# Optimization experiments

Hardware: AMD Instinct MI355X
Metric: run time of the kernel (lower is better)

The kernel has to match this reference:

```python
import jax, jax.numpy as jnp
import numpy as np

B, S, H, SSZ, IN = 1024, 100, 128, 100, 2


def _gru(x, h, Wih, Whh, bih, bhh):
    # PyTorch GRU cell: gates ordered (reset, update, new)
    gx = x @ Wih.T + bih
    gh = h @ Whh.T + bhh
    xr, xz, xn = jnp.split(gx, 3, axis=-1)
    hr, hz, hn = jnp.split(gh, 3, axis=-1)
    r = jax.nn.sigmoid(xr + hr)
    z = jax.nn.sigmoid(xz + hz)
    n = jnp.tanh(xn + r * hn)
    return (1.0 - z) * n + z * h


def _attn(inst_h, rnn_out, W, v):
    # inst_h: [B,S,H], rnn_out: [B,H] -> softmax attention weights [B,S]
    h = jnp.concatenate([inst_h, jnp.broadcast_to(rnn_out[:, None, :], inst_h.shape)], axis=-1)
    s = jax.nn.relu(jnp.einsum('bsk,kh->bsh', h, W)) @ v
    return jax.nn.softmax(s, axis=1)


def setup_inputs() -> dict:
    key = jax.random.key(0)
    k = jax.random.split(key, 32)
    p = lambda i, shape, sc=0.05: sc * jax.random.normal(k[i], shape, jnp.float32)
    instance = jax.random.uniform(k[0], (B, S, IN), jnp.float32)
    # solutions must be per-row permutations of node indices
    solution_1 = jnp.argsort(jax.random.uniform(k[1], (B, S)), axis=1).astype(jnp.int32)
    solution_2 = jnp.argsort(jax.random.uniform(k[2], (B, S)), axis=1).astype(jnp.int32)
    eps = jax.random.normal(k[3], (B, SSZ), jnp.float32)
    return dict(
        instance=instance, solution_1=solution_1, solution_2=solution_2, eps=eps,
        emb_i_W=p(4, (H, IN)), emb_i_b=jnp.zeros(H, jnp.float32),
        emb_r_W=p(5, (H, IN)), emb_r_b=jnp.zeros(H, jnp.float32),
        attn_W=p(6, (2 * H, H)), attn_v=p(7, (H,)),
        gru_Wih=p(8, (3 * H, H)), gru_Whh=p(9, (3 * H, H)),
        gru_bih=jnp.zeros(3 * H, jnp.float32), gru_bhh=jnp.zeros(3 * H, jnp.float32),
        grud_Wih=p(10, (3 * H, 2 * H)), grud_Whh=p(11, (3 * H, H)),
        grud_bih=jnp.zeros(3 * H, jnp.float32), grud_bhh=jnp.zeros(3 * H, jnp.float32),
        enc_fc1_W=p(12, (SSZ, H)), enc_fc1_b=jnp.zeros(SSZ, jnp.float32),
        enc_fc2_W=p(13, (SSZ, H)), enc_fc2_b=jnp.zeros(SSZ, jnp.float32),
        ptr_W=p(14, (2 * H, H)), ptr_v=p(15, (H,)),
        pfc1_W=p(16, (2 * H, 2 * H + SSZ)), pfc1_b=jnp.zeros(2 * H, jnp.float32),
        pfc2_W=p(17, (H, 2 * H)), pfc2_b=jnp.zeros(H, jnp.float32),
    )


def reference(instance, solution_1, solution_2, eps,
              emb_i_W, emb_i_b, emb_r_W, emb_r_b, attn_W, attn_v,
              gru_Wih, gru_Whh, gru_bih, gru_bhh,
              grud_Wih, grud_Whh, grud_bih, grud_bhh,
              enc_fc1_W, enc_fc1_b, enc_fc2_W, enc_fc2_b,
              ptr_W, ptr_v, pfc1_W, pfc1_b, pfc2_W, pfc2_b):
    b_idx = jnp.arange(B)
    inst_h = instance @ emb_i_W.T + emb_i_b  # [B,S,H]
    emb_r = lambda x: x @ emb_r_W.T + emb_r_b
    take = lambda ptr: instance[b_idx, ptr]  # gather node coords [B,IN]

    # ---------------- Encoder ----------------
    def enc_step(carry, ptr):
        h1, h2, ref_h = carry
        h1 = _gru(ref_h, h1, gru_Wih, gru_Whh, gru_bih, gru_bhh)
        a = _attn(inst_h, h1, attn_W, attn_v)
        context = jnp.einsum('bs,bsh->bh', a, inst_h)
        ref_h = emb_r(take(ptr))
        rnn_in = jnp.concatenate([ref_h, context], axis=-1)  # [B,2H]
        h2 = _gru(rnn_in, h2, grud_Wih, grud_Whh, grud_bih, grud_bhh)
        return (h1, h2, ref_h), None

    z0 = jnp.zeros((B, H), instance.dtype)
    ref_h0 = emb_r(take(solution_1[:, 0]))
    (_, h2, _), _ = jax.lax.scan(enc_step, (z0, z0, ref_h0), solution_1[:, 1:].T)
    mu = h2 @ enc_fc1_W.T + enc_fc1_b
    log_var = h2 @ enc_fc2_W.T + enc_fc2_b
    Z = mu + eps * jnp.exp(0.5 * log_var)

    # ---------------- Decoder (teacher forcing) ----------------
    mask0 = jnp.ones((B, S), instance.dtype).at[b_idx, solution_2[:, 0]].set(0.0)

    def dec_step(carry, ptr):
        h1, ref_in, mask = carry
        ref_h = emb_r(ref_in)
        h1 = _gru(ref_h, h1, gru_Wih, gru_Whh, gru_bih, gru_bhh)
        a = _attn(inst_h, h1, attn_W, attn_v)
        context = jnp.einsum('bs,bsh->bh', a, inst_h)
        fc_in = jnp.concatenate([context, Z, ref_h], axis=-1)  # [B, 2H+SSZ]
        fc_out = (fc_in @ pfc1_W.T + pfc1_b) @ pfc2_W.T + pfc2_b  # no activation, as in torch
        hcat = jnp.concatenate([inst_h, jnp.broadcast_to(fc_out[:, None, :], inst_h.shape)], axis=-1)
        logits = jnp.tanh(jnp.einsum('bsk,kh->bsh', hcat, ptr_W)) @ ptr_v  # [B,S]
        probs = jax.nn.softmax(logits + jnp.log(mask), axis=1)
        logp = jnp.log(probs[b_idx, ptr])
        pred = jnp.argmax(probs, axis=1)
        mask = mask.at[b_idx, ptr].set(0.0)  # tsp.update_mask: mark chosen node visited
        return (h1, take(ptr), mask), (pred, logp)

    init = (z0, take(solution_2[:, 0]), mask0)
    _, (preds, logps) = jax.lax.scan(dec_step, init, solution_2[:, 1:].T)
    tour_idx = jnp.concatenate([solution_2[:, :1], preds.T.astype(solution_2.dtype)], axis=1)
    tour_logp = logps.T  # [B, S-1]
    return (mu, log_var, Z, tour_idx, tour_logp)
```

## Files before the change

kernel.cpp:

```cpp
#include <hip/hip_runtime.h>
#include <math.h>

static constexpr int NB  = 1024;
static constexpr int NS  = 100;
static constexpr int NH  = 128;
static constexpr int GPB = 2;
static constexpr int NTHR = 256;
static constexpr int NBLK = NB / GPB;

static constexpr int OUT_MU = 0;
static constexpr int OUT_LV = NB * NS;
static constexpr int OUT_Z  = 2 * NB * NS;
static constexpr int OUT_TI = 3 * NB * NS;
static constexpr int OUT_LP = 4 * NB * NS;

#define NEGF (-3.4e38f)

template<int C4>
__device__ __forceinline__ void dot2x3f(const float* __restrict__ wr0,
        const float* __restrict__ wr1, const float* __restrict__ wr2,
        const float* __restrict__ x0, const float* __restrict__ x1,
        float& r00, float& r01, float& r10, float& r11, float& r20, float& r21)
{
    const float4* W0 = reinterpret_cast<const float4*>(wr0);
    const float4* W1 = reinterpret_cast<const float4*>(wr1);
    const float4* W2 = reinterpret_cast<const float4*>(wr2);
    const float4* X0 = reinterpret_cast<const float4*>(x0);
    const float4* X1 = reinterpret_cast<const float4*>(x1);
    float a00 = 0.f, a01 = 0.f, a10 = 0.f, a11 = 0.f, a20 = 0.f, a21 = 0.f;
    #pragma unroll 8
    for (int c = 0; c < C4; ++c) {
        float4 u0 = W0[c], u1 = W1[c], u2 = W2[c];
        float4 v0 = X0[c], v1 = X1[c];
        a00 = fmaf(u0.x, v0.x, a00); a00 = fmaf(u0.y, v0.y, a00); a00 = fmaf(u0.z, v0.z, a00); a00 = fmaf(u0.w, v0.w, a00);
        a01 = fmaf(u0.x, v1.x, a01); a01 = fmaf(u0.y, v1.y, a01); a01 = fmaf(u0.z, v1.z, a01); a01 = fmaf(u0.w, v1.w, a01);
        a10 = fmaf(u1.x, v0.x, a10); a10 = fmaf(u1.y, v0.y, a10); a10 = fmaf(u1.z, v0.z, a10); a10 = fmaf(u1.w, v0.w, a10);
        a11 = fmaf(u1.x, v1.x, a11); a11 = fmaf(u1.y, v1.y, a11); a11 = fmaf(u1.z, v1.z, a11); a11 = fmaf(u1.w, v1.w, a11);
        a20 = fmaf(u2.x, v0.x, a20); a20 = fmaf(u2.y, v0.y, a20); a20 = fmaf(u2.z, v0.z, a20); a20 = fmaf(u2.w, v0.w, a20);
        a21 = fmaf(u2.x, v1.x, a21); a21 = fmaf(u2.y, v1.y, a21); a21 = fmaf(u2.z, v1.z, a21); a21 = fmaf(u2.w, v1.w, a21);
    }
    r00 = a00; r01 = a01; r10 = a10; r11 = a11; r20 = a20; r21 = a21;
}

template<int C4>
__device__ __forceinline__ void dot2f(const float* __restrict__ w,
        const float* __restrict__ x0, const float* __restrict__ x1, float& r0, float& r1)
{
    const float4* W = reinterpret_cast<const float4*>(w);
    const float4* X0 = reinterpret_cast<const float4*>(x0);
    const float4* X1 = reinterpret_cast<const float4*>(x1);
    float a0 = 0.f, a1 = 0.f;
    #pragma unroll 8
    for (int c = 0; c < C4; ++c) {
        float4 u = W[c];
        float4 v0 = X0[c], v1 = X1[c];
        a0 = fmaf(u.x, v0.x, a0); a0 = fmaf(u.y, v0.y, a0); a0 = fmaf(u.z, v0.z, a0); a0 = fmaf(u.w, v0.w, a0);
        a1 = fmaf(u.x, v1.x, a1); a1 = fmaf(u.y, v1.y, a1); a1 = fmaf(u.z, v1.z, a1); a1 = fmaf(u.w, v1.w, a1);
    }
    r0 = a0; r1 = a1;
}

template<int C4>
__device__ __forceinline__ void dot1f(const float* __restrict__ w,
        const float* __restrict__ x0, float& r0)
{
    const float4* W = reinterpret_cast<const float4*>(w);
    const float4* X0 = reinterpret_cast<const float4*>(x0);
    float a0 = 0.f;
    #pragma unroll 8
    for (int c = 0; c < C4; ++c) {
        float4 u = W[c];
        float4 v0 = X0[c];
        a0 = fmaf(u.x, v0.x, a0); a0 = fmaf(u.y, v0.y, a0); a0 = fmaf(u.z, v0.z, a0); a0 = fmaf(u.w, v0.w, a0);
    }
    r0 = a0;
}

template<int C4>
__device__ __forceinline__ double dotwd(const float* __restrict__ w, const float* __restrict__ x)
{
    const float4* W = reinterpret_cast<const float4*>(w);
    double a = 0.0;
    #pragma unroll 8
    for (int c = 0; c < C4; ++c) {
        float4 u = W[c];
        const float* p = x + 4 * c;
        a = fma((double)u.x, (double)p[0], a);
        a = fma((double)u.y, (double)p[1], a);
        a = fma((double)u.z, (double)p[2], a);
        a = fma((double)u.w, (double)p[3], a);
    }
    return a;
}

__device__ __forceinline__ void gruc(const float* __restrict__ bih, const float* __restrict__ bhh,
        const float* __restrict__ pa, const float* __restrict__ pb, float* __restrict__ h, int j)
{
    double r = 1.0 / (1.0 + exp(-(((double)pa[j]        + (double)bih[j])        + ((double)pb[j]        + (double)bhh[j]))));
    double z = 1.0 / (1.0 + exp(-(((double)pa[NH + j]   + (double)bih[NH + j])   + ((double)pb[NH + j]   + (double)bhh[NH + j]))));
    double n = tanh(((double)pa[2*NH + j] + (double)bih[2*NH + j]) + r * ((double)pb[2*NH + j] + (double)bhh[2*NH + j]));
    h[j] = (float)((1.0 - z) * n + z * (double)h[j]);
}

__global__ __launch_bounds__(NTHR) void vae_v14(
    const float* __restrict__ instance, const int* __restrict__ sol1,
    const int* __restrict__ sol2, const float* __restrict__ eps,
    const float* __restrict__ emb_i_W, const float* __restrict__ emb_i_b,
    const float* __restrict__ emb_r_W, const float* __restrict__ emb_r_b,
    const float* __restrict__ attn_W, const float* __restrict__ attn_v,
    const float* __restrict__ gru_Wih, const float* __restrict__ gru_Whh,
    const float* __restrict__ gru_bih, const float* __restrict__ gru_bhh,
    const float* __restrict__ grud_Wih, const float* __restrict__ grud_Whh,
    const float* __restrict__ grud_bih, const float* __restrict__ grud_bhh,
    const float* __restrict__ efc1_W, const float* __restrict__ efc1_b,
    const float* __restrict__ efc2_W, const float* __restrict__ efc2_b,
    const float* __restrict__ ptr_W, const float* __restrict__ ptr_v,
    const float* __restrict__ pfc1_W, const float* __restrict__ pfc1_b,
    const float* __restrict__ pfc2_W, const float* __restrict__ pfc2_b,
    float* __restrict__ out)
{
    __shared__ float  s_x[GPB][360];
    __shared__ float  s_h1[GPB][NH], s_h2[GPB][NH], s_fco[GPB][NH];
    __shared__ float  s_fch[GPB][256];
    __shared__ float  s_pa[GPB][3 * NH], s_pb[GPB][3 * NH];
    __shared__ double s_qh[GPB][NH];
    __shared__ double s_qpA[GPB][NH], s_qpB[GPB][NH];
    __shared__ double2 dAa[NH], dAp[NH];
    __shared__ double dAba[NH], dAbp[NH];
    __shared__ float  s_lg[GPB][NS], s_a[GPB][NS];
    __shared__ float  s_c0[GPB][NS], s_c1[GPB][NS], s_msk[GPB][NS];
    __shared__ float  t_wi0[NH], t_wi1[NH], t_bi[NH];
    __shared__ float  t_wr0[NH], t_wr1[NH], t_br[NH];
    __shared__ float  t_va[NH], t_vp[NH];
    __shared__ float  t_gbih[3*NH], t_gbhh[3*NH], t_dbih[3*NH], t_dbhh[3*NH];
    __shared__ float  t_p1b[256], t_p2b[NH];
    __shared__ int    s_sol1[GPB][NS], s_sol2[GPB][NS];
    __shared__ float  s_red[GPB][2];
    __shared__ double s_redd[GPB][2];
    __shared__ int    s_ri[GPB][2];
    __shared__ float  s_rc0[GPB], s_rc1[GPB];

    const int tid = threadIdx.x;
    const int bbase = blockIdx.x * GPB;
    const int j = tid & (NH - 1);
    const int half = tid >> 7;
    const int g = half;
    const int lane = tid & 63;
    const int wid = (tid >> 6) & 1;

    if (tid < NH) {
        t_wi0[tid] = emb_i_W[2*tid]; t_wi1[tid] = emb_i_W[2*tid+1]; t_bi[tid] = emb_i_b[tid];
        t_wr0[tid] = emb_r_W[2*tid]; t_wr1[tid] = emb_r_W[2*tid+1]; t_br[tid] = emb_r_b[tid];
        t_va[tid] = attn_v[tid]; t_vp[tid] = ptr_v[tid];
        t_p2b[tid] = pfc2_b[tid];
    }
    t_p1b[tid] = pfc1_b[tid];
    for (int i = tid; i < 3 * NH; i += NTHR) {
        t_gbih[i] = gru_bih[i]; t_gbhh[i] = gru_bhh[i];
        t_dbih[i] = grud_bih[i]; t_dbhh[i] = grud_bhh[i];
    }
    for (int i = tid; i < GPB * NS; i += NTHR) {
        int gg = i / NS, s = i - gg * NS;
        s_c0[gg][s] = instance[(size_t)((bbase + gg) * NS + s) * 2 + 0];
        s_c1[gg][s] = instance[(size_t)((bbase + gg) * NS + s) * 2 + 1];
        s_sol1[gg][s] = sol1[(bbase + gg) * NS + s];
        s_sol2[gg][s] = sol2[(bbase + gg) * NS + s];
    }
    s_h1[g][j] = 0.f;
    s_h2[g][j] = 0.f;
    __syncthreads();
    {
        const float* Wm = (half == 0) ? attn_W : ptr_W;
        double a0 = 0.0, a1 = 0.0, ab = 0.0;
        for (int k = 0; k < NH; ++k) {
            double wv = (double)Wm[(size_t)k * NH + j];
            a0 = fma((double)t_wi0[k], wv, a0);
            a1 = fma((double)t_wi1[k], wv, a1);
            ab = fma((double)t_bi[k],  wv, ab);
        }
        if (half == 0) { dAa[j].x = a0; dAa[j].y = a1; dAba[j] = ab; }
        else           { dAp[j].x = a0; dAp[j].y = a1; dAbp[j] = ab; }
    }
    {
        int sp = s_sol1[g][0];
        s_x[g][j] = fmaf(s_c0[g][sp], t_wr0[j], fmaf(s_c1[g][sp], t_wr1[j], t_br[j]));
    }
    __syncthreads();

    for (int t = 1; t < NS; ++t) {
        if (half == 0) {
            float a00,a01,a10,a11,a20,a21;
            dot2x3f<32>(gru_Wih + (size_t)j * NH, gru_Wih + (size_t)(NH + j) * NH,
                        gru_Wih + (size_t)(2*NH + j) * NH, s_x[0], s_x[1],
                        a00,a01,a10,a11,a20,a21);
            s_pa[0][j] = a00;        s_pa[1][j] = a01;
            s_pa[0][NH + j] = a10;   s_pa[1][NH + j] = a11;
            s_pa[0][2*NH + j] = a20; s_pa[1][2*NH + j] = a21;
        } else {
            float a00,a01,a10,a11,a20,a21;
            dot2x3f<32>(gru_Whh + (size_t)j * NH, gru_Whh + (size_t)(NH + j) * NH,
                        gru_Whh + (size_t)(2*NH + j) * NH, s_h1[0], s_h1[1],
                        a00,a01,a10,a11,a20,a21);
            s_pb[0][j] = a00;        s_pb[1][j] = a01;
            s_pb[0][NH + j] = a10;   s_pb[1][NH + j] = a11;
            s_pb[0][2*NH + j] = a20; s_pb[1][2*NH + j] = a21;
        }
        __syncthreads();
        gruc(t_gbih, t_gbhh, s_pa[g], s_pb[g], s_h1[g], j);
        __syncthreads();
        {
            const float* col = attn_W + (size_t)NH * NH + j;
            const int k0 = half * 64;
            double a00=0.0,a01=0.0,a02=0.0,a03=0.0;
            double a10=0.0,a11=0.0,a12=0.0,a13=0.0;
            #pragma unroll 8
            for (int k = 0; k < 64; k += 4) {
                float w0 = col[(size_t)(k0+k+0) * NH];
                float w1 = col[(size_t)(k0+k+1) * NH];
                float w2 = col[(size_t)(k0+k+2) * NH];
                float w3 = col[(size_t)(k0+k+3) * NH];
                float4 h0 = *reinterpret_cast<const float4*>(&s_h1[0][k0+k]);
                float4 h1v = *reinterpret_cast<const float4*>(&s_h1[1][k0+k]);
                a00 = fma((double)w0, (double)h0.x, a00);
                a01 = fma((double)w1, (double)h0.y, a01);
                a02 = fma((double)w2, (double)h0.z, a02);
                a03 = fma((double)w3, (double)h0.w, a03);
                a10 = fma((double)w0, (double)h1v.x, a10);
                a11 = fma((double)w1, (double)h1v.y, a11);
                a12 = fma((double)w2, (double)h1v.z, a12);
                a13 = fma((double)w3, (double)h1v.w, a13);
            }
            if (half == 0) { s_qpA[0][j] = (a00+a01)+(a02+a03); s_qpA[1][j] = (a10+a11)+(a12+a13); }
            else           { s_qpB[0][j] = (a00+a01)+(a02+a03); s_qpB[1][j] = (a10+a11)+(a12+a13); }
        }
        __syncthreads();
        s_qh[g][j] = dAba[j] + (s_qpA[g][j] + s_qpB[g][j]);
        __syncthreads();
        if (j < NS) {
            double c00 = (double)s_c0[g][j], c10 = (double)s_c1[g][j];
            double acc0 = 0.0, acc1 = 0.0, acc2 = 0.0, acc3 = 0.0;
            #pragma unroll 4
            for (int h = 0; h < NH; h += 4) {
                double2 A0 = dAa[h+0], A1 = dAa[h+1], A2 = dAa[h+2], A3 = dAa[h+3];
                double p0 = fma(c00, A0.x, fma(c10, A0.y, s_qh[g][h+0]));
                double p1 = fma(c00, A1.x, fma(c10, A1.y, s_qh[g][h+1]));
                double p2 = fma(c00, A2.x, fma(c10, A2.y, s_qh[g][h+2]));
                double p3 = fma(c00, A3.x, fma(c10, A3.y, s_qh[g][h+3]));
                acc0 = fma(fmax(p0, 0.0), (double)t_va[h+0], acc0);
                acc1 = fma(fmax(p1, 0.0), (double)t_va[h+1], acc1);
                acc2 = fma(fmax(p2, 0.0), (double)t_va[h+2], acc2);
                acc3 = fma(fmax(p3, 0.0), (double)t_va[h+3], acc3);
            }
            s_lg[g][j] = (float)(((acc0 + acc1) + (acc2 + acc3)));
        }
        __syncthreads();
        {
            float a = s_lg[g][lane];
            float b = (lane + 64 < NS) ? s_lg[g][lane + 64] : NEGF;
            float m = fmaxf(a, b);
            m = fmaxf(m, __shfl_xor(m, 32)); m = fmaxf(m, __shfl_xor(m, 16));
            m = fmaxf(m, __shfl_xor(m, 8));  m = fmaxf(m, __shfl_xor(m, 4));
            m = fmaxf(m, __shfl_xor(m, 2));  m = fmaxf(m, __shfl_xor(m, 1));
            float fv = 0.f;
            if (j < NS) { fv = (float)exp((double)s_lg[g][j] - (double)m); s_a[g][j] = fv; }
            double ps = (double)fv;
            ps += __shfl_xor(ps, 32); ps += __shfl_xor(ps, 16);
            ps += __shfl_xor(ps, 8);  ps += __shfl_xor(ps, 4);
            ps += __shfl_xor(ps, 2);  ps += __shfl_xor(ps, 1);
            if (lane == 0) s_redd[g][wid] = ps;
        }
        __syncthreads();
        if (j < NS) {
            double se = s_redd[g][0] + s_redd[g][1];
            s_a[g][j] = (float)((double)s_a[g][j] / se);
        }
        __syncthreads();
        {
            float w0 = t_wi0[j], w1 = t_wi1[j], bb = t_bi[j];
            double a0 = 0.0, a1 = 0.0, a2 = 0.0, a3 = 0.0;
            #pragma unroll 5
            for (int s = 0; s < NS; s += 4) {
                float ih0 = fmaf(s_c0[g][s+0], w0, fmaf(s_c1[g][s+0], w1, bb));
                float ih1 = fmaf(s_c0[g][s+1], w0, fmaf(s_c1[g][s+1], w1, bb));
                float ih2 = fmaf(s_c0[g][s+2], w0, fmaf(s_c1[g][s+2], w1, bb));
                float ih3 = fmaf(s_c0[g][s+3], w0, fmaf(s_c1[g][s+3], w1, bb));
                a0 += (double)s_a[g][s+0] * (double)ih0;
                a1 += (double)s_a[g][s+1] * (double)ih1;
                a2 += (double)s_a[g][s+2] * (double)ih2;
                a3 += (double)s_a[g][s+3] * (double)ih3;
            }
            s_x[g][NH + j] = (float)(((a0 + a1) + (a2 + a3)));
            int sp = s_sol1[g][t];
            s_x[g][j] = fmaf(s_c0[g][sp], t_wr0[j], fmaf(s_c1[g][sp], t_wr1[j], t_br[j]));
        }
        __syncthreads();
        if (half == 0) {
            float a00,a01,a10,a11,a20,a21;
            dot2x3f<64>(grud_Wih + (size_t)j * 256, grud_Wih + (size_t)(NH + j) * 256,
                        grud_Wih + (size_t)(2*NH + j) * 256, s_x[0], s_x[1],
                        a00,a01,a10,a11,a20,a21);
            s_pa[0][j] = a00;        s_pa[1][j] = a01;
            s_pa[0][NH + j] = a10;   s_pa[1][NH + j] = a11;
            s_pa[0][2*NH + j] = a20; s_pa[1][2*NH + j] = a21;
        } else {
            float a00,a01,a10,a11,a20,a21;
            dot2x3f<32>(grud_Whh + (size_t)j * NH, grud_Whh + (size_t)(NH + j) * NH,
                        grud_Whh + (size_t)(2*NH + j) * NH, s_h2[0], s_h2[1],
                        a00,a01,a10,a11,a20,a21);
            s_pb[0][j] = a00;        s_pb[1][j] = a01;
            s_pb[0][NH + j] = a10;   s_pb[1][NH + j] = a11;
            s_pb[0][2*NH + j] = a20; s_pb[1][2*NH + j] = a21;
        }
        __syncthreads();
        gruc(t_dbih, t_dbhh, s_pa[g], s_pb[g], s_h2[g], j);
        __syncthreads();
    }

    for (int idx = tid; idx < GPB * NS; idx += NTHR) {
        int gg = idx / NS, s = idx - gg * NS, b = bbase + gg;
        double mu = dotwd<32>(efc1_W + (size_t)s * NH, s_h2[gg]) + (double)efc1_b[s];
        double lv = dotwd<32>(efc2_W + (size_t)s * NH, s_h2[gg]) + (double)efc2_b[s];
        double z  = mu + (double)eps[(size_t)b * NS + s] * exp(0.5 * lv);
        out[OUT_MU + b * NS + s] = (float)mu;
        out[OUT_LV + b * NS + s] = (float)lv;
        out[OUT_Z  + b * NS + s] = (float)z;
        s_x[gg][NH + s] = (float)z;
    }
    for (int i = tid; i < GPB * NS; i += NTHR) {
        int gg = i / NS, s = i - gg * NS;
        s_msk[gg][s] = 1.f;
    }
    s_h1[g][j] = 0.f;
    __syncthreads();
    if (tid < GPB) {
        int b = bbase + tid;
        int s0 = s_sol2[tid][0];
        s_msk[tid][s0] = 0.f;
        s_rc0[tid] = s_c0[tid][s0];
        s_rc1[tid] = s_c1[tid][s0];
        out[OUT_TI + b * NS + 0] = (float)s0;
    }
    __syncthreads();

    for (int t = 1; t < NS; ++t) {
        s_x[g][228 + j] = fmaf(s_rc0[g], t_wr0[j], fmaf(s_rc1[g], t_wr1[j], t_br[j]));
        __syncthreads();
        if (half == 0) {
            float a00,a01,a10,a11,a20,a21;
            dot2x3f<32>(gru_Wih + (size_t)j * NH, gru_Wih + (size_t)(NH + j) * NH,
                        gru_Wih + (size_t)(2*NH + j) * NH, s_x[0]+228, s_x[1]+228,
                        a00,a01,a10,a11,a20,a21);
            s_pa[0][j] = a00;        s_pa[1][j] = a01;
            s_pa[0][NH + j] = a10;   s_pa[1][NH + j] = a11;
            s_pa[0][2*NH + j] = a20; s_pa[1][2*NH + j] = a21;
        } else {
            float a00,a01,a10,a11,a20,a21;
            dot2x3f<32>(gru_Whh + (size_t)j * NH, gru_Whh + (size_t)(NH + j) * NH,
                        gru_Whh + (size_t)(2*NH + j) * NH, s_h1[0], s_h1[1],
                        a00,a01,a10,a11,a20,a21);
            s_pb[0][j] = a00;        s_pb[1][j] = a01;
            s_pb[0][NH + j] = a10;   s_pb[1][NH + j] = a11;
            s_pb[0][2*NH + j] = a20; s_pb[1][2*NH + j] = a21;
        }
        __syncthreads();
        gruc(t_gbih, t_gbhh, s_pa[g], s_pb[g], s_h1[g], j);
        __syncthreads();
        {
            const float* col = attn_W + (size_t)NH * NH + j;
            const int k0 = half * 64;
            double a00=0.0,a01=0.0,a02=0.0,a03=0.0;
            double a10=0.0,a11=0.0,a12=0.0,a13=0.0;
            #pragma unroll 8
            for (int k = 0; k < 64; k += 4) {
                float w0 = col[(size_t)(k0+k+0) * NH];
                float w1 = col[(size_t)(k0+k+1) * NH];
                float w2 = col[(size_t)(k0+k+2) * NH];
                float w3 = col[(size_t)(k0+k+3) * NH];
                float4 h0 = *reinterpret_cast<const float4*>(&s_h1[0][k0+k]);
                float4 h1v = *reinterpret_cast<const float4*>(&s_h1[1][k0+k]);
                a00 = fma((double)w0, (double)h0.x, a00);
                a01 = fma((double)w1, (double)h0.y, a01);
                a02 = fma((double)w2, (double)h0.z, a02);
                a03 = fma((double)w3, (double)h0.w, a03);
                a10 = fma((double)w0, (double)h1v.x, a10);
                a11 = fma((double)w1, (double)h1v.y, a11);
                a12 = fma((double)w2, (double)h1v.z, a12);
                a13 = fma((double)w3, (double)h1v.w, a13);
            }
            if (half == 0) { s_qpA[0][j] = (a00+a01)+(a02+a03); s_qpA[1][j] = (a10+a11)+(a12+a13); }
            else           { s_qpB[0][j] = (a00+a01)+(a02+a03); s_qpB[1][j] = (a10+a11)+(a12+a13); }
        }
        __syncthreads();
        s_qh[g][j] = dAba[j] + (s_qpA[g][j] + s_qpB[g][j]);
        __syncthreads();
        if (j < NS) {
            double c00 = (double)s_c0[g][j], c10 = (double)s_c1[g][j];
            double acc0 = 0.0, acc1 = 0.0, acc2 = 0.0, acc3 = 0.0;
            #pragma unroll 4
            for (int h = 0; h < NH; h += 4) {
                double2 A0 = dAa[h+0], A1 = dAa[h+1], A2 = dAa[h+2], A3 = dAa[h+3];
                double p0 = fma(c00, A0.x, fma(c10, A0.y, s_qh[g][h+0]));
                double p1 = fma(c00, A1.x, fma(c10, A1.y, s_qh[g][h+1]));
                double p2 = fma(c00, A2.x, fma(c10, A2.y, s_qh[g][h+2]));
                double p3 = fma(c00, A3.x, fma(c10, A3.y, s_qh[g][h+3]));
                acc0 = fma(fmax(p0, 0.0), (double)t_va[h+0], acc0);
                acc1 = fma(fmax(p1, 0.0), (double)t_va[h+1], acc1);
                acc2 = fma(fmax(p2, 0.0), (double)t_va[h+2], acc2);
                acc3 = fma(fmax(p3, 0.0), (double)t_va[h+3], acc3);
            }
            s_lg[g][j] = (float)(((acc0 + acc1) + (acc2 + acc3)));
        }
        __syncthreads();
        {
            float a = s_lg[g][lane];
            float b = (lane + 64 < NS) ? s_lg[g][lane + 64] : NEGF;
            float m = fmaxf(a, b);
            m = fmaxf(m, __shfl_xor(m, 32)); m = fmaxf(m, __shfl_xor(m, 16));
            m = fmaxf(m, __shfl_xor(m, 8));  m = fmaxf(m, __shfl_xor(m, 4));
            m = fmaxf(m, __shfl_xor(m, 2));  m = fmaxf(m, __shfl_xor(m, 1));
            float fv = 0.f;
            if (j < NS) { fv = (float)exp((double)s_lg[g][j] - (double)m); s_a[g][j] = fv; }
            double ps = (double)fv;
            ps += __shfl_xor(ps, 32); ps += __shfl_xor(ps, 16);
            ps += __shfl_xor(ps, 8);  ps += __shfl_xor(ps, 4);
            ps += __shfl_xor(ps, 2);  ps += __shfl_xor(ps, 1);
            if (lane == 0) s_redd[g][wid] = ps;
        }
        __syncthreads();
        if (j < NS) {
            double se = s_redd[g][0] + s_redd[g][1];
            s_a[g][j] = (float)((double)s_a[g][j] / se);
        }
        __syncthreads();
        {
            float w0 = t_wi0[j], w1 = t_wi1[j], bb = t_bi[j];
            double a0 = 0.0, a1 = 0.0, a2 = 0.0, a3 = 0.0;
            #pragma unroll 5
            for (int s = 0; s < NS; s += 4) {
                float ih0 = fmaf(s_c0[g][s+0], w0, fmaf(s_c1[g][s+0], w1, bb));
                float ih1 = fmaf(s_c0[g][s+1], w0, fmaf(s_c1[g][s+1], w1, bb));
                float ih2 = fmaf(s_c0[g][s+2], w0, fmaf(s_c1[g][s+2], w1, bb));
                float ih3 = fmaf(s_c0[g][s+3], w0, fmaf(s_c1[g][s+3], w1, bb));
                a0 += (double)s_a[g][s+0] * (double)ih0;
                a1 += (double)s_a[g][s+1] * (double)ih1;
                a2 += (double)s_a[g][s+2] * (double)ih2;
                a3 += (double)s_a[g][s+3] * (double)ih3;
            }
            s_x[g][j] = (float)(((a0 + a1) + (a2 + a3)));
        }
        __syncthreads();
        {
            float r0, r1;
            dot2f<89>(pfc1_W + (size_t)tid * 356, s_x[0], s_x[1], r0, r1);
            float bb = t_p1b[tid];
            s_fch[0][tid] = r0 + bb; s_fch[1][tid] = r1 + bb;
        }
        __syncthreads();
        {
            float r0;
            dot1f<64>(pfc2_W + (size_t)j * 256, s_fch[g], r0);
            s_fco[g][j] = r0 + t_p2b[j];
        }
        __syncthreads();
        {
            const float* col = ptr_W + (size_t)NH * NH + j;
            const int k0 = half * 64;
            double a00=0.0,a01=0.0,a02=0.0,a03=0.0;
            double a10=0.0,a11=0.0,a12=0.0,a13=0.0;
            #pragma unroll 8
            for (int k = 0; k < 64; k += 4) {
                float w0 = col[(size_t)(k0+k+0) * NH];
                float w1 = col[(size_t)(k0+k+1) * NH];
                float w2 = col[(size_t)(k0+k+2) * NH];
                float w3 = col[(size_t)(k0+k+3) * NH];
                float4 f0 = *reinterpret_cast<const float4*>(&s_fco[0][k0+k]);
                float4 f1 = *reinterpret_cast<const float4*>(&s_fco[1][k0+k]);
                a00 = fma((double)w0, (double)f0.x, a00);
                a01 = fma((double)w1, (double)f0.y, a01);
                a02 = fma((double)w2, (double)f0.z, a02);
                a03 = fma((double)w3, (double)f0.w, a03);
                a10 = fma((double)w0, (double)f1.x, a10);
                a11 = fma((double)w1, (double)f1.y, a11);
                a12 = fma((double)w2, (double)f1.z, a12);
                a13 = fma((double)w3, (double)f1.w, a13);
            }
            if (half == 0) { s_qpA[0][j] = (a00+a01)+(a02+a03); s_qpA[1][j] = (a10+a11)+(a12+a13); }
            else           { s_qpB[0][j] = (a00+a01)+(a02+a03); s_qpB[1][j] = (a10+a11)+(a12+a13); }
        }
        __syncthreads();
        s_qh[g][j] = dAbp[j] + (s_qpA[g][j] + s_qpB[g][j]);
        __syncthreads();
        if (j < NS) {
            double c00 = (double)s_c0[g][j], c10 = (double)s_c1[g][j];
            double acc0 = 0.0, acc1 = 0.0, acc2 = 0.0, acc3 = 0.0;
            #pragma unroll 4
            for (int h = 0; h < NH; h += 4) {
                double2 A0 = dAp[h+0], A1 = dAp[h+1], A2 = dAp[h+2], A3 = dAp[h+3];
                double p0 = fma(c00, A0.x, fma(c10, A0.y, s_qh[g][h+0]));
                double p1 = fma(c00, A1.x, fma(c10, A1.y, s_qh[g][h+1]));
                double p2 = fma(c00, A2.x, fma(c10, A2.y, s_qh[g][h+2]));
                double p3 = fma(c00, A3.x, fma(c10, A3.y, s_qh[g][h+3]));
                acc0 = fma((double)tanhf((float)p0), (double)t_vp[h+0], acc0);
                acc1 = fma((double)tanhf((float)p1), (double)t_vp[h+1], acc1);
                acc2 = fma((double)tanhf((float)p2), (double)t_vp[h+2], acc2);
                acc3 = fma((double)tanhf((float)p3), (double)t_vp[h+3], acc3);
            }
            s_lg[g][j] = (float)(((acc0 + acc1) + (acc2 + acc3)));
        }
        __syncthreads();
        {
            float la = s_lg[g][lane];
            float ma = (s_msk[g][lane] > 0.f) ? la : NEGF;
            float lb = NEGF;
            if (lane + 64 < NS) lb = (s_msk[g][lane + 64] > 0.f) ? s_lg[g][lane + 64] : NEGF;
            float m = fmaxf(ma, lb);
            m = fmaxf(m, __shfl_xor(m, 32)); m = fmaxf(m, __shfl_xor(m, 16));
            m = fmaxf(m, __shfl_xor(m, 8));  m = fmaxf(m, __shfl_xor(m, 4));
            m = fmaxf(m, __shfl_xor(m, 2));  m = fmaxf(m, __shfl_xor(m, 1));
            float fv = 0.f;
            if (j < NS) {
                fv = (s_msk[g][j] > 0.f) ? (float)exp((double)s_lg[g][j] - (double)m) : 0.f;
                s_a[g][j] = fv;
            }
            float  bv = (j < NS) ? fv : -1.f;
            int    bi = (j < NS) ? j  : NS;
            double ps = (j < NS) ? (double)fv : 0.0;
            #pragma unroll
            for (int o = 32; o >= 1; o >>= 1) {
                float  ov = __shfl_xor(bv, o);
                int    oi = __shfl_xor(bi, o);
                double op = __shfl_xor(ps, o);
                ps += op;
                if (ov > bv || (ov == bv && oi < bi)) { bv = ov; bi = oi; }
            }
            if (lane == 0) { s_red[g][wid] = bv; s_ri[g][wid] = bi; s_redd[g][wid] = ps; }
        }
        __syncthreads();
        if (tid < GPB) {
            int gg = tid, b = bbase + gg;
            float m = -1.f; int mi = NS; double se = 0.0;
            for (int i = 0; i < 2; ++i) {
                se += s_redd[gg][i];
                float v = s_red[gg][i]; int vi = s_ri[gg][i];
                if (v > m || (v == m && vi < mi)) { m = v; mi = vi; }
            }
            int pt = s_sol2[gg][t];
            double logp = log((double)s_a[gg][pt] / se);
            out[OUT_TI + b * NS + t]             = (float)mi;
            out[OUT_LP + b * (NS - 1) + (t - 1)] = (float)logp;
            s_msk[gg][pt] = 0.f;
            s_rc0[gg] = s_c0[gg][pt];
            s_rc1[gg] = s_c1[gg][pt];
        }
        __syncthreads();
    }
}

extern "C" void kernel_launch(void* const* d_in, const int* in_sizes, int n_in,
                              void* d_out, int out_size, void* d_ws, size_t ws_size,
                              hipStream_t stream)
{
    (void)in_sizes; (void)n_in; (void)out_size; (void)d_ws; (void)ws_size;
    vae_v14<<<NBLK, NTHR, 0, stream>>>(
        (const float*)d_in[0], (const int*)d_in[1], (const int*)d_in[2], (const float*)d_in[3],
        (const float*)d_in[4], (const float*)d_in[5], (const float*)d_in[6], (const float*)d_in[7],
        (const float*)d_in[8], (const float*)d_in[9], (const float*)d_in[10], (const float*)d_in[11],
        (const float*)d_in[12], (const float*)d_in[13], (const float*)d_in[14], (const float*)d_in[15],
        (const float*)d_in[16], (const float*)d_in[17], (const float*)d_in[18], (const float*)d_in[19],
        (const float*)d_in[20], (const float*)d_in[21], (const float*)d_in[22], (const float*)d_in[23],
        (const float*)d_in[24], (const float*)d_in[25], (const float*)d_in[26], (const float*)d_in[27],
        (float*)d_out);
}
```

Measured before the change: 12.26 ms.

## Defer decoder GRU update into next step and cut per-step barriers

The encoder's second GRU update is moved to the start of the next timestep. Its hidden-state matvec now runs on the idle half-block alongside the first GRU's gate update, and each thread handles one group's input matvec. This removes two barriers per encoder step. Softmax and argmax reductions are merged into single-wave per-group reductions that write normalized weights directly, and the separate q-vector staging pass is folded into the logits loop. Together these drop several __syncthreads per step, at the cost of recomputing the q sums per thread and more complex control flow.

```diff
diff --git a/kernel.cpp b/kernel.cpp
--- a/kernel.cpp
+++ b/kernel.cpp
@@ -28,7 +28,7 @@
     const float4* X0 = reinterpret_cast<const float4*>(x0);
     const float4* X1 = reinterpret_cast<const float4*>(x1);
     float a00 = 0.f, a01 = 0.f, a10 = 0.f, a11 = 0.f, a20 = 0.f, a21 = 0.f;
-    #pragma unroll 8
+    #pragma unroll 4
     for (int c = 0; c < C4; ++c) {
         float4 u0 = W0[c], u1 = W1[c], u2 = W2[c];
         float4 v0 = X0[c], v1 = X1[c];
@@ -40,6 +40,27 @@
         a21 = fmaf(u2.x, v1.x, a21); a21 = fmaf(u2.y, v1.y, a21); a21 = fmaf(u2.z, v1.z, a21); a21 = fmaf(u2.w, v1.w, a21);
     }
     r00 = a00; r01 = a01; r10 = a10; r11 = a11; r20 = a20; r21 = a21;
+}
+
+template<int C4>
+__device__ __forceinline__ void dot1x3f(const float* __restrict__ wr0,
+        const float* __restrict__ wr1, const float* __restrict__ wr2,
+        const float* __restrict__ x, float& r0, float& r1, float& r2)
+{
+    const float4* W0 = reinterpret_cast<const float4*>(wr0);
+    const float4* W1 = reinterpret_cast<const float4*>(wr1);
+    const float4* W2 = reinterpret_cast<const float4*>(wr2);
+    const float4* X  = reinterpret_cast<const float4*>(x);
+    float a0 = 0.f, a1 = 0.f, a2 = 0.f;
+    #pragma unroll 4
+    for (int c = 0; c < C4; ++c) {
+        float4 u0 = W0[c], u1 = W1[c], u2 = W2[c];
+        float4 v = X[c];
+        a0 = fmaf(u0.x, v.x, a0); a0 = fmaf(u0.y, v.y, a0); a0 = fmaf(u0.z, v.z, a0); a0 = fmaf(u0.w, v.w, a0);
+        a1 = fmaf(u1.x, v.x, a1); a1 = fmaf(u1.y, v.y, a1); a1 = fmaf(u1.z, v.z, a1); a1 = fmaf(u1.w, v.w, a1);
+        a2 = fmaf(u2.x, v.x, a2); a2 = fmaf(u2.y, v.y, a2); a2 = fmaf(u2.z, v.z, a2); a2 = fmaf(u2.w, v.w, a2);
+    }
+    r0 = a0; r1 = a1; r2 = a2;
 }
 
 template<int C4>
@@ -102,7 +123,7 @@
     h[j] = (float)((1.0 - z) * n + z * (double)h[j]);
 }
 
-__global__ __launch_bounds__(NTHR) void vae_v14(
+__global__ __launch_bounds__(NTHR) void vae_v18(
     const float* __restrict__ instance, const int* __restrict__ sol1,
     const int* __restrict__ sol2, const float* __restrict__ eps,
     const float* __restrict__ emb_i_W, const float* __restrict__ emb_i_b,
@@ -123,7 +144,7 @@
     __shared__ float  s_h1[GPB][NH], s_h2[GPB][NH], s_fco[GPB][NH];
     __shared__ float  s_fch[GPB][256];
     __shared__ float  s_pa[GPB][3 * NH], s_pb[GPB][3 * NH];
-    __shared__ double s_qh[GPB][NH];
+    __shared__ float  s_pa2[GPB][3 * NH], s_pb2[GPB][3 * NH];
     __shared__ double s_qpA[GPB][NH], s_qpB[GPB][NH];
     __shared__ double2 dAa[NH], dAp[NH];
     __shared__ double dAba[NH], dAbp[NH];
@@ -135,10 +156,6 @@
     __shared__ float  t_gbih[3*NH], t_gbhh[3*NH], t_dbih[3*NH], t_dbhh[3*NH];
     __shared__ float  t_p1b[256], t_p2b[NH];
     __shared__ int    s_sol1[GPB][NS], s_sol2[GPB][NS];
-    __shared__ float  s_red[GPB][2];
-    __shared__ double s_redd[GPB][2];
-    __shared__ int    s_ri[GPB][2];
-    __shared__ float  s_rc0[GPB], s_rc1[GPB];
 
     const int tid = threadIdx.x;
     const int bbase = blockIdx.x * GPB;
@@ -147,6 +164,7 @@
     const int g = half;
     const int lane = tid & 63;
     const int wid = (tid >> 6) & 1;
+    const int k0 = half * 64;
 
     if (tid < NH) {
         t_wi0[tid] = emb_i_W[2*tid]; t_wi1[tid] = emb_i_W[2*tid+1]; t_bi[tid] = emb_i_b[tid];
@@ -173,10 +191,10 @@
         const float* Wm = (half == 0) ? attn_W : ptr_W;
         double a0 = 0.0, a1 = 0.0, ab = 0.0;
         for (int k = 0; k < NH; ++k) {
-            double wv = (double)Wm[(size_t)k * NH + j];
-            a0 = fma((double)t_wi0[k], wv, a0);
-            a1 = fma((double)t_wi1[k], wv, a1);
-            ab = fma((double)t_bi[k],  wv, ab);
+            double wv2 = (double)Wm[(size_t)k * NH + j];
+            a0 = fma((double)t_wi0[k], wv2, a0);
+            a1 = fma((double)t_wi1[k], wv2, a1);
+            ab = fma((double)t_bi[k],  wv2, ab);
         }
         if (half == 0) { dAa[j].x = a0; dAa[j].y = a1; dAba[j] = ab; }
         else           { dAp[j].x = a0; dAp[j].y = a1; dAbp[j] = ab; }
@@ -188,6 +206,7 @@
     __syncthreads();
 
     for (int t = 1; t < NS; ++t) {
+        if (t > 1) gruc(t_dbih, t_dbhh, s_pa2[g], s_pb2[g], s_h2[g], j);
         if (half == 0) {
             float a00,a01,a10,a11,a20,a21;
             dot2x3f<32>(gru_Wih + (size_t)j * NH, gru_Wih + (size_t)(NH + j) * NH,
@@ -207,10 +226,18 @@
         }
         __syncthreads();
         gruc(t_gbih, t_gbhh, s_pa[g], s_pb[g], s_h1[g], j);
+        if (half == 1) {
+            float a00,a01,a10,a11,a20,a21;
+            dot2x3f<32>(grud_Whh + (size_t)j * NH, grud_Whh + (size_t)(NH + j) * NH,
+                        grud_Whh + (size_t)(2*NH + j) * NH, s_h2[0], s_h2[1],
+                        a00,a01,a10,a11,a20,a21);
+            s_pb2[0][j] = a00;        s_pb2[1][j] = a01;
+            s_pb2[0][NH + j] = a10;   s_pb2[1][NH + j] = a11;
+            s_pb2[0][2*NH + j] = a20; s_pb2[1][2*NH + j] = a21;
+        }
         __syncthreads();
         {
             const float* col = attn_W + (size_t)NH * NH + j;
-            const int k0 = half * 64;
             double a00=0.0,a01=0.0,a02=0.0,a03=0.0;
             double a10=0.0,a11=0.0,a12=0.0,a13=0.0;
             #pragma unroll 8
@@ -234,18 +261,20 @@
             else           { s_qpB[0][j] = (a00+a01)+(a02+a03); s_qpB[1][j] = (a10+a11)+(a12+a13); }
         }
         __syncthreads();
-        s_qh[g][j] = dAba[j] + (s_qpA[g][j] + s_qpB[g][j]);
-        __syncthreads();
         if (j < NS) {
             double c00 = (double)s_c0[g][j], c10 = (double)s_c1[g][j];
             double acc0 = 0.0, acc1 = 0.0, acc2 = 0.0, acc3 = 0.0;
             #pragma unroll 4
             for (int h = 0; h < NH; h += 4) {
                 double2 A0 = dAa[h+0], A1 = dAa[h+1], A2 = dAa[h+2], A3 = dAa[h+3];
-                double p0 = fma(c00, A0.x, fma(c10, A0.y, s_qh[g][h+0]));
-                double p1 = fma(c00, A1.x, fma(c10, A1.y, s_qh[g][h+1]));
-                double p2 = fma(c00, A2.x, fma(c10, A2.y, s_qh[g][h+2]));
-                double p3 = fma(c00, A3.x, fma(c10, A3.y, s_qh[g][h+3]));
+                double q0 = dAba[h+0] + (s_qpA[g][h+0] + s_qpB[g][h+0]);
+                double q1 = dAba[h+1] + (s_qpA[g][h+1] + s_qpB[g][h+1]);
+                double q2v= dAba[h+2] + (s_qpA[g][h+2] + s_qpB[g][h+2]);
+                double q3 = dAba[h+3] + (s_qpA[g][h+3] + s_qpB[g][h+3]);
+                double p0 = fma(c00, A0.x, fma(c10, A0.y, q0));
+                double p1 = fma(c00, A1.x, fma(c10, A1.y, q1));
+                double p2 = fma(c00, A2.x, fma(c10, A2.y, q2v));
+                double p3 = fma(c00, A3.x, fma(c10, A3.y, q3));
                 acc0 = fma(fmax(p0, 0.0), (double)t_va[h+0], acc0);
                 acc1 = fma(fmax(p1, 0.0), (double)t_va[h+1], acc1);
                 acc2 = fma(fmax(p2, 0.0), (double)t_va[h+2], acc2);
@@ -254,25 +283,23 @@
             s_lg[g][j] = (float)(((acc0 + acc1) + (acc2 + acc3)));
         }
         __syncthreads();
-        {
-            float a = s_lg[g][lane];
-            float b = (lane + 64 < NS) ? s_lg[g][lane + 64] : NEGF;
-            float m = fmaxf(a, b);
+        if (tid < 128) {
+            const int gg = wid;
+            float v1 = s_lg[gg][lane];
+            float v2 = (lane + 64 < NS) ? s_lg[gg][lane + 64] : NEGF;
+            float m = fmaxf(v1, v2);
             m = fmaxf(m, __shfl_xor(m, 32)); m = fmaxf(m, __shfl_xor(m, 16));
             m = fmaxf(m, __shfl_xor(m, 8));  m = fmaxf(m, __shfl_xor(m, 4));
             m = fmaxf(m, __shfl_xor(m, 2));  m = fmaxf(m, __shfl_xor(m, 1));
-            float fv = 0.f;
-            if (j < NS) { fv = (float)exp((double)s_lg[g][j] - (double)m); s_a[g][j] = fv; }
-            double ps = (double)fv;
+            float f1 = (float)exp((double)v1 - (double)m);
+            float f2 = 0.f;
+            if (lane + 64 < NS) f2 = (float)exp((double)v2 - (double)m);
+            double ps = (double)f1 + (double)f2;
             ps += __shfl_xor(ps, 32); ps += __shfl_xor(ps, 16);
             ps += __shfl_xor(ps, 8);  ps += __shfl_xor(ps, 4);
             ps += __shfl_xor(ps, 2);  ps += __shfl_xor(ps, 1);
-            if (lane == 0) s_redd[g][wid] = ps;
-        }
-        __syncthreads();
-        if (j < NS) {
-            double se = s_redd[g][0] + s_redd[g][1];
-            s_a[g][j] = (float)((double)s_a[g][j] / se);
+            s_a[gg][lane] = (float)((double)f1 / ps);
+            if (lane + 64 < NS) s_a[gg][lane + 64] = (float)((double)f2 / ps);
         }
         __syncthreads();
         {
@@ -294,27 +321,16 @@
             s_x[g][j] = fmaf(s_c0[g][sp], t_wr0[j], fmaf(s_c1[g][sp], t_wr1[j], t_br[j]));
         }
         __syncthreads();
-        if (half == 0) {
-            float a00,a01,a10,a11,a20,a21;
-            dot2x3f<64>(grud_Wih + (size_t)j * 256, grud_Wih + (size_t)(NH + j) * 256,
-                        grud_Wih + (size_t)(2*NH + j) * 256, s_x[0], s_x[1],
-                        a00,a01,a10,a11,a20,a21);
-            s_pa[0][j] = a00;        s_pa[1][j] = a01;
-            s_pa[0][NH + j] = a10;   s_pa[1][NH + j] = a11;
-            s_pa[0][2*NH + j] = a20; s_pa[1][2*NH + j] = a21;
-        } else {
-            float a00,a01,a10,a11,a20,a21;
-            dot2x3f<32>(grud_Whh + (size_t)j * NH, grud_Whh + (size_t)(NH + j) * NH,
-                        grud_Whh + (size_t)(2*NH + j) * NH, s_h2[0], s_h2[1],
-                        a00,a01,a10,a11,a20,a21);
-            s_pb[0][j] = a00;        s_pb[1][j] = a01;
-            s_pb[0][NH + j] = a10;   s_pb[1][NH + j] = a11;
-            s_pb[0][2*NH + j] = a20; s_pb[1][2*NH + j] = a21;
-        }
-        __syncthreads();
-        gruc(t_dbih, t_dbhh, s_pa[g], s_pb[g], s_h2[g], j);
-        __syncthreads();
-    }
+        {
+            float r0, r1, r2;
+            dot1x3f<64>(grud_Wih + (size_t)j * 256, grud_Wih + (size_t)(NH + j) * 256,
+                        grud_Wih + (size_t)(2*NH + j) * 256, s_x[g], r0, r1, r2);
+            s_pa2[g][j] = r0; s_pa2[g][NH + j] = r1; s_pa2[g][2*NH + j] = r2;
+        }
+        __syncthreads();
+    }
+    gruc(t_dbih, t_dbhh, s_pa2[g], s_pb2[g], s_h2[g], j);
+    __syncthreads();
 
     for (int idx = tid; idx < GPB * NS; idx += NTHR) {
         int gg = idx / NS, s = idx - gg * NS, b = bbase + gg;
@@ -331,20 +347,20 @@
         s_msk[gg][s] = 1.f;
     }
     s_h1[g][j] = 0.f;
+    {
+        int pt = s_sol2[g][0];
+        s_x[g][228 + j] = fmaf(s_c0[g][pt], t_wr0[j], fmaf(s_c1[g][pt], t_wr1[j], t_br[j]));
+    }
     __syncthreads();
     if (tid < GPB) {
         int b = bbase + tid;
         int s0 = s_sol2[tid][0];
         s_msk[tid][s0] = 0.f;
-        s_rc0[tid] = s_c0[tid][s0];
-        s_rc1[tid] = s_c1[tid][s0];
         out[OUT_TI + b * NS + 0] = (float)s0;
     }
     __syncthreads();
 
     for (int t = 1; t < NS; ++t) {
-        s_x[g][228 + j] = fmaf(s_rc0[g], t_wr0[j], fmaf(s_rc1[g], t_wr1[j], t_br[j]));
-        __syncthreads();
         if (half == 0) {
             float a00,a01,a10,a11,a20,a21;
             dot2x3f<32>(gru_Wih + (size_t)j * NH, gru_Wih + (size_t)(NH + j) * NH,
@@ -367,7 +383,6 @@
         __syncthreads();
         {
             const float* col = attn_W + (size_t)NH * NH + j;
-            const int k0 = half * 64;
             double a00=0.0,a01=0.0,a02=0.0,a03=0.0;
             double a10=0.0,a11=0.0,a12=0.0,a13=0.0;
             #pragma unroll 8
@@ -391,18 +406,20 @@
             else           { s_qpB[0][j] = (a00+a01)+(a02+a03); s_qpB[1][j] = (a10+a11)+(a12+a13); }
         }
         __syncthreads();
-        s_qh[g][j] = dAba[j] + (s_qpA[g][j] + s_qpB[g][j]);
-        __syncthreads();
         if (j < NS) {
             double c00 = (double)s_c0[g][j], c10 = (double)s_c1[g][j];
             double acc0 = 0.0, acc1 = 0.0, acc2 = 0.0, acc3 = 0.0;
             #pragma unroll 4
             for (int h = 0; h < NH; h += 4) {
                 double2 A0 = dAa[h+0], A1 = dAa[h+1], A2 = dAa[h+2], A3 = dAa[h+3];
-                double p0 = fma(c00, A0.x, fma(c10, A0.y, s_qh[g][h+0]));
-                double p1 = fma(c00, A1.x, fma(c10, A1.y, s_qh[g][h+1]));
-                double p2 = fma(c00, A2.x, fma(c10, A2.y, s_qh[g][h+2]));
-                double p3 = fma(c00, A3.x, fma(c10, A3.y, s_qh[g][h+3]));
+                double q0 = dAba[h+0] + (s_qpA[g][h+0] + s_qpB[g][h+0]);
+                double q1 = dAba[h+1] + (s_qpA[g][h+1] + s_qpB[g][h+1]);
+                double q2v= dAba[h+2] + (s_qpA[g][h+2] + s_qpB[g][h+2]);
+                double q3 = dAba[h+3] + (s_qpA[g][h+3] + s_qpB[g][h+3]);
+                double p0 = fma(c00, A0.x, fma(c10, A0.y, q0));
+                double p1 = fma(c00, A1.x, fma(c10, A1.y, q1));
+                double p2 = fma(c00, A2.x, fma(c10, A2.y, q2v));
+                double p3 = fma(c00, A3.x, fma(c10, A3.y, q3));
                 acc0 = fma(fmax(p0, 0.0), (double)t_va[h+0], acc0);
                 acc1 = fma(fmax(p1, 0.0), (double)t_va[h+1], acc1);
                 acc2 = fma(fmax(p2, 0.0), (double)t_va[h+2], acc2);
@@ -411,25 +428,23 @@
             s_lg[g][j] = (float)(((acc0 + acc1) + (acc2 + acc3)));
         }
         __syncthreads();
-        {
-            float a = s_lg[g][lane];
-            float b = (lane + 64 < NS) ? s_lg[g][lane + 64] : NEGF;
-            float m = fmaxf(a, b);
+        if (tid < 128) {
+            const int gg = wid;
+            float v1 = s_lg[gg][lane];
+            float v2 = (lane + 64 < NS) ? s_lg[gg][lane + 64] : NEGF;
+            float m = fmaxf(v1, v2);
             m = fmaxf(m, __shfl_xor(m, 32)); m = fmaxf(m, __shfl_xor(m, 16));
             m = fmaxf(m, __shfl_xor(m, 8));  m = fmaxf(m, __shfl_xor(m, 4));
             m = fmaxf(m, __shfl_xor(m, 2));  m = fmaxf(m, __shfl_xor(m, 1));
-            float fv = 0.f;
-            if (j < NS) { fv = (float)exp((double)s_lg[g][j] - (double)m); s_a[g][j] = fv; }
-            double ps = (double)fv;
+            float f1 = (float)exp((double)v1 - (double)m);
+            float f2 = 0.f;
+            if (lane + 64 < NS) f2 = (float)exp((double)v2 - (double)m);
+            double ps = (double)f1 + (double)f2;
             ps += __shfl_xor(ps, 32); ps += __shfl_xor(ps, 16);
             ps += __shfl_xor(ps, 8);  ps += __shfl_xor(ps, 4);
             ps += __shfl_xor(ps, 2);  ps += __shfl_xor(ps, 1);
-            if (lane == 0) s_redd[g][wid] = ps;
-        }
-        __syncthreads();
-        if (j < NS) {
-            double se = s_redd[g][0] + s_redd[g][1];
-            s_a[g][j] = (float)((double)s_a[g][j] / se);
+            s_a[gg][lane] = (float)((double)f1 / ps);
+            if (lane + 64 < NS) s_a[gg][lane + 64] = (float)((double)f2 / ps);
         }
         __syncthreads();
         {
@@ -464,7 +479,6 @@
         __syncthreads();
         {
             const float* col = ptr_W + (size_t)NH * NH + j;
-            const int k0 = half * 64;
             double a00=0.0,a01=0.0,a02=0.0,a03=0.0;
             double a10=0.0,a11=0.0,a12=0.0,a13=0.0;
             #pragma unroll 8
@@ -488,18 +502,20 @@
             else           { s_qpB[0][j] = (a00+a01)+(a02+a03); s_qpB[1][j] = (a10+a11)+(a12+a13); }
         }
         __syncthreads();
-        s_qh[g][j] = dAbp[j] + (s_qpA[g][j] + s_qpB[g][j]);
-        __syncthreads();
         if (j < NS) {
             double c00 = (double)s_c0[g][j], c10 = (double)s_c1[g][j];
             double acc0 = 0.0, acc1 = 0.0, acc2 = 0.0, acc3 = 0.0;
             #pragma unroll 4
             for (int h = 0; h < NH; h += 4) {
                 double2 A0 = dAp[h+0], A1 = dAp[h+1], A2 = dAp[h+2], A3 = dAp[h+3];
-                double p0 = fma(c00, A0.x, fma(c10, A0.y, s_qh[g][h+0]));
-                double p1 = fma(c00, A1.x, fma(c10, A1.y, s_qh[g][h+1]));
-                double p2 = fma(c00, A2.x, fma(c10, A2.y, s_qh[g][h+2]));
-                double p3 = fma(c00, A3.x, fma(c10, A3.y, s_qh[g][h+3]));
+                double q0 = dAbp[h+0] + (s_qpA[g][h+0] + s_qpB[g][h+0]);
+                double q1 = dAbp[h+1] + (s_qpA[g][h+1] + s_qpB[g][h+1]);
+                double q2v= dAbp[h+2] + (s_qpA[g][h+2] + s_qpB[g][h+2]);
+                double q3 = dAbp[h+3] + (s_qpA[g][h+3] + s_qpB[g][h+3]);
+                double p0 = fma(c00, A0.x, fma(c10, A0.y, q0));
+                double p1 = fma(c00, A1.x, fma(c10, A1.y, q1));
+                double p2 = fma(c00, A2.x, fma(c10, A2.y, q2v));
+                double p3 = fma(c00, A3.x, fma(c10, A3.y, q3));
                 acc0 = fma((double)tanhf((float)p0), (double)t_vp[h+0], acc0);
                 acc1 = fma((double)tanhf((float)p1), (double)t_vp[h+1], acc1);
                 acc2 = fma((double)tanhf((float)p2), (double)t_vp[h+2], acc2);
@@ -508,23 +524,23 @@
             s_lg[g][j] = (float)(((acc0 + acc1) + (acc2 + acc3)));
         }
         __syncthreads();
-        {
-            float la = s_lg[g][lane];
-            float ma = (s_msk[g][lane] > 0.f) ? la : NEGF;
-            float lb = NEGF;
-            if (lane + 64 < NS) lb = (s_msk[g][lane + 64] > 0.f) ? s_lg[g][lane + 64] : NEGF;
-            float m = fmaxf(ma, lb);
+        if (tid < 128) {
+            const int gg = wid;
+            const int j1 = lane, j2 = lane + 64;
+            float l1 = s_lg[gg][j1];
+            bool  u1 = s_msk[gg][j1] > 0.f;
+            float c1v = u1 ? l1 : NEGF;
+            float l2 = 0.f; bool u2 = false; float c2v = NEGF;
+            if (j2 < NS) { l2 = s_lg[gg][j2]; u2 = s_msk[gg][j2] > 0.f; c2v = u2 ? l2 : NEGF; }
+            float m = fmaxf(c1v, c2v);
             m = fmaxf(m, __shfl_xor(m, 32)); m = fmaxf(m, __shfl_xor(m, 16));
             m = fmaxf(m, __shfl_xor(m, 8));  m = fmaxf(m, __shfl_xor(m, 4));
             m = fmaxf(m, __shfl_xor(m, 2));  m = fmaxf(m, __shfl_xor(m, 1));
-            float fv = 0.f;
-            if (j < NS) {
-                fv = (s_msk[g][j] > 0.f) ? (float)exp((double)s_lg[g][j] - (double)m) : 0.f;
-                s_a[g][j] = fv;
-            }
-            float  bv = (j < NS) ? fv : -1.f;
-            int    bi = (j < NS) ? j  : NS;
-            double ps = (j < NS) ? (double)fv : 0.0;
+            float f1 = u1 ? (float)exp((double)l1 - (double)m) : 0.f;
+            float f2 = (j2 < NS && u2) ? (float)exp((double)l2 - (double)m) : 0.f;
+            float bv = f1; int bi = j1;
+            if (j2 < NS && f2 > bv) { bv = f2; bi = j2; }
+            double ps = (double)f1 + (double)f2;
             #pragma unroll
             for (int o = 32; o >= 1; o >>= 1) {
                 float  ov = __shfl_xor(bv, o);
@@ -533,24 +549,24 @@
                 ps += op;
                 if (ov > bv || (ov == bv && oi < bi)) { bv = ov; bi = oi; }
             }
-            if (lane == 0) { s_red[g][wid] = bv; s_ri[g][wid] = bi; s_redd[g][wid] = ps; }
-        }
-        __syncthreads();
-        if (tid < GPB) {
-            int gg = tid, b = bbase + gg;
-            float m = -1.f; int mi = NS; double se = 0.0;
-            for (int i = 0; i < 2; ++i) {
-                se += s_redd[gg][i];
-                float v = s_red[gg][i]; int vi = s_ri[gg][i];
-                if (v > m || (v == m && vi < mi)) { m = v; mi = vi; }
-            }
             int pt = s_sol2[gg][t];
-            double logp = log((double)s_a[gg][pt] / se);
-            out[OUT_TI + b * NS + t]             = (float)mi;
-            out[OUT_LP + b * (NS - 1) + (t - 1)] = (float)logp;
-            s_msk[gg][pt] = 0.f;
-            s_rc0[gg] = s_c0[gg][pt];
-            s_rc1[gg] = s_c1[gg][pt];
+            float a1s = __shfl(f1, pt & 63);
+            float a2s = __shfl(f2, pt & 63);
+            float a_pt = (pt < 64) ? a1s : a2s;
+            if (lane == 0) {
+                int b2 = bbase + gg;
+                double logp = log((double)a_pt / ps);
+                out[OUT_TI + b2 * NS + t]             = (float)bi;
+                out[OUT_LP + b2 * (NS - 1) + (t - 1)] = (float)logp;
+                s_msk[gg][pt] = 0.f;
+            }
+        } else {
+            const int i = tid - 128;
+            #pragma unroll
+            for (int gg = 0; gg < GPB; ++gg) {
+                int pt = s_sol2[gg][t];
+                s_x[gg][228 + i] = fmaf(s_c0[gg][pt], t_wr0[i], fmaf(s_c1[gg][pt], t_wr1[i], t_br[i]));
+            }
         }
         __syncthreads();
     }
@@ -561,7 +577,7 @@
                               hipStream_t stream)
 {
     (void)in_sizes; (void)n_in; (void)out_size; (void)d_ws; (void)ws_size;
-    vae_v14<<<NBLK, NTHR, 0, stream>>>(
+    vae_v18<<<NBLK, NTHR, 0, stream>>>(
         (const float*)d_in[0], (const int*)d_in[1], (const int*)d_in[2], (const float*)d_in[3],
         (const float*)d_in[4], (const float*)d_in[5], (const float*)d_in[6], (const float*)d_in[7],
         (const float*)d_in[8], (const float*)d_in[9], (const float*)d_in[10], (const float*)d_in[11],
```

New measurement: 14.53 ms. +18.5%, slower.
